# Optimization experiments

Measured on AMD Instinct MI355X. Metric: run time of the kernel, lower is better.

## Reference

```python
import jax, jax.numpy as jnp
import numpy as np
import math

CHANNELS = 128
NUM_NODES = 170
LENGTH = 12
BATCH = 128


def setup_inputs() -> dict:
    key = jax.random.key(0)
    k_x, k_es = jax.random.split(key)
    x = jax.random.normal(k_x, (BATCH, CHANNELS, NUM_NODES, LENGTH), dtype=jnp.float32)
    # xavier_uniform for E_s [channels, num_nodes]
    bound = math.sqrt(6.0 / (CHANNELS + NUM_NODES))
    E_s = jax.random.uniform(k_es, (CHANNELS, NUM_NODES), dtype=jnp.float32,
                             minval=-bound, maxval=bound)
    return {"x": x, "E_s": E_s}


def reference(x, E_s):
    # x: [B, C, N, T], E_s: [C, M] with M == N (num_nodes)
    # Note: the original also computes E_t = x * E_tod**2, which is dead code
    # (never used in the returned value), so it is omitted here.
    C = x.shape[1]
    # node embeddings: sum over channel and time -> [B, N, M]
    E_d = jnp.tanh(jnp.einsum('bcnt,cm->bnm', x, E_s))
    # node-node similarity: contract over the M (embedding) axis -> [B, N, N]
    scores = jax.nn.relu(jnp.einsum('bnm,bkm->bnk', E_d, E_d) / jnp.sqrt(jnp.float32(C)))
    A_adp = jax.nn.softmax(scores, axis=-1)  # [B, N, N]
    A_mean = A_adp.mean(axis=0)              # [N, N]
    return (A_mean > 0.5).astype(jnp.float32)
```

## Files before the change

### kernel.cpp

```cpp
#include <hip/hip_runtime.h>
#include <math.h>

#define NB 128
#define NC 128
#define NN 170
#define NT 12
#define MP 176
#define BSROW 196

#define XS_SZ  (NB * NC * MP)
#define ESP_SZ (NC * MP)
#define P_SZ   (NB * NN * MP)
#define ED_SZ  (NB * NN * MP)

__global__ __launch_bounds__(256) void k1_reduce_pad(const float* __restrict__ x,
                                                     const float* __restrict__ Es,
                                                     float* __restrict__ xs,
                                                     float* __restrict__ Esp) {
    if (blockIdx.x >= 10880) {
        int idx = (blockIdx.x - 10880) * 256 + threadIdx.x;
        if (idx < ESP_SZ) {
            int c = idx / MP, m = idx % MP;
            Esp[idx] = (m < NN) ? Es[c * NN + m] : 0.f;
        }
        return;
    }
    const int w    = blockIdx.x * 4 + (threadIdx.x >> 6);
    const int lane = threadIdx.x & 63;
    const float4* x4 = reinterpret_cast<const float4*>(x) + (size_t)w * 192;
    float4 f0 = x4[lane], f1 = x4[lane + 64], f2 = x4[lane + 128];
    float p0 = (f0.x + f0.y) + (f0.z + f0.w);
    float p1 = (f1.x + f1.y) + (f1.z + f1.w);
    float p2 = (f2.x + f2.y) + (f2.z + f2.w);
    float tot = 0.f;
    #pragma unroll
    for (int j = 0; j < 3; ++j) {
        int s = 3 * lane + j;
        int src = s & 63, reg = s >> 6;
        float a0 = __shfl(p0, src, 64);
        float a1 = __shfl(p1, src, 64);
        float a2 = __shfl(p2, src, 64);
        tot += (reg == 0) ? a0 : (reg == 1) ? a1 : a2;
    }
    int g  = w * 64 + lane;
    int bc = g / NN, n = g - bc * NN;
    xs[(size_t)bc * MP + n] = tot;
    if (n < MP - NN) xs[(size_t)bc * MP + NN + n] = 0.f;
}

__global__ __launch_bounds__(256) void k2_embed(const float* __restrict__ xs,
                                                const float* __restrict__ Esp,
                                                float* __restrict__ Ed) {
    const int b = blockIdx.y, n0 = blockIdx.x * 32;
    const int t = threadIdx.x, tx = t & 15, ty = t >> 4;
    __shared__ __align__(16) float As[16][36];
    __shared__ __align__(16) float Bs[16][BSROW];

    float acc[2][12] = {};
    for (int c0 = 0; c0 < NC; c0 += 16) {
        __syncthreads();
        if (t < 128) {
            int c = t >> 3, q = t & 7;
            float4 v = *reinterpret_cast<const float4*>(
                xs + ((size_t)(b * NC + c0 + c)) * MP + n0 + q * 4);
            *reinterpret_cast<float4*>(&As[c][q * 4]) = v;
        }
        #pragma unroll
        for (int it = 0; it < 3; ++it) {
            int idx = t + it * 256;
            int c = idx / 48, mq = idx - c * 48;
            float4 v = make_float4(0.f, 0.f, 0.f, 0.f);
            if (mq < 44)
                v = *reinterpret_cast<const float4*>(Esp + (c0 + c) * MP + mq * 4);
            *reinterpret_cast<float4*>(&Bs[c][mq * 4]) = v;
        }
        __syncthreads();
        #pragma unroll
        for (int cc = 0; cc < 16; ++cc) {
            float2 av = *reinterpret_cast<const float2*>(&As[cc][ty * 2]);
            float a[2] = {av.x, av.y};
            float bb[12];
            #pragma unroll
            for (int off = 0; off < 3; ++off) {
                float4 bv = *reinterpret_cast<const float4*>(&Bs[cc][tx * 4 + off * 64]);
                bb[off * 4 + 0] = bv.x; bb[off * 4 + 1] = bv.y;
                bb[off * 4 + 2] = bv.z; bb[off * 4 + 3] = bv.w;
            }
            #pragma unroll
            for (int ii = 0; ii < 2; ++ii)
                #pragma unroll
                for (int jj = 0; jj < 12; ++jj)
                    acc[ii][jj] = fmaf(a[ii], bb[jj], acc[ii][jj]);
        }
    }
    #pragma unroll
    for (int ii = 0; ii < 2; ++ii) {
        int n = n0 + ty * 2 + ii;
        if (n >= NN) continue;
        float* Erow = Ed + ((size_t)(b * NN + n)) * MP;
        #pragma unroll
        for (int off = 0; off < 3; ++off) {
            int m = tx * 4 + off * 64;
            if (m >= MP) continue;
            float4 v;
            v.x = tanhf(acc[ii][off * 4 + 0]);
            v.y = tanhf(acc[ii][off * 4 + 1]);
            v.z = tanhf(acc[ii][off * 4 + 2]);
            v.w = tanhf(acc[ii][off * 4 + 3]);
            *reinterpret_cast<float4*>(Erow + m) = v;
        }
    }
}

__global__ __launch_bounds__(256) void k3_scores(const float* __restrict__ Ed,
                                                 float* __restrict__ P) {
    const int b = blockIdx.y, r0 = blockIdx.x * 32;
    const int t = threadIdx.x, tx = t & 15, ty = t >> 4;
    __shared__ __align__(16) float Bs[16][BSROW];
    const float* __restrict__ Edb = Ed + (size_t)b * NN * MP;

    float acc[2][12] = {};
    for (int mc = 0; mc < MP; mc += 16) {
        __syncthreads();
        #pragma unroll
        for (int it = 0; it < 3; ++it) {
            int idx = t + it * 256;
            int k = idx >> 2, mq = idx & 3;
            float4 v = make_float4(0.f, 0.f, 0.f, 0.f);
            if (k < NN)
                v = *reinterpret_cast<const float4*>(Edb + (size_t)k * MP + mc + mq * 4);
            Bs[mq * 4 + 0][k] = v.x;
            Bs[mq * 4 + 1][k] = v.y;
            Bs[mq * 4 + 2][k] = v.z;
            Bs[mq * 4 + 3][k] = v.w;
        }
        __syncthreads();
        #pragma unroll
        for (int mm = 0; mm < 16; ++mm) {
            float2 av = *reinterpret_cast<const float2*>(&Bs[mm][r0 + ty * 2]);
            float a[2] = {av.x, av.y};
            float bb[12];
            #pragma unroll
            for (int off = 0; off < 3; ++off) {
                float4 bv = *reinterpret_cast<const float4*>(&Bs[mm][tx * 4 + off * 64]);
                bb[off * 4 + 0] = bv.x; bb[off * 4 + 1] = bv.y;
                bb[off * 4 + 2] = bv.z; bb[off * 4 + 3] = bv.w;
            }
            #pragma unroll
            for (int ii = 0; ii < 2; ++ii)
                #pragma unroll
                for (int jj = 0; jj < 12; ++jj)
                    acc[ii][jj] = fmaf(a[ii], bb[jj], acc[ii][jj]);
        }
    }

    const float scale = 0.08838834764831845f;
    #pragma unroll
    for (int ii = 0; ii < 2; ++ii) {
        int n = r0 + ty * 2 + ii;
        float vv[12];
        float mx = -1.f;
        #pragma unroll
        for (int jj = 0; jj < 12; ++jj) {
            int k = tx * 4 + (jj & 3) + (jj >> 2) * 64;
            bool valid = (k < NN);
            float v = fmaxf(acc[ii][jj] * scale, 0.f);
            vv[jj] = valid ? v : -1.f;
            mx = fmaxf(mx, vv[jj]);
        }
        #pragma unroll
        for (int off = 8; off; off >>= 1) mx = fmaxf(mx, __shfl_xor(mx, off, 64));
        float ex[12], sum = 0.f;
        #pragma unroll
        for (int jj = 0; jj < 12; ++jj) {
            int k = tx * 4 + (jj & 3) + (jj >> 2) * 64;
            float e = (k < NN) ? __expf(vv[jj] - mx) : 0.f;
            ex[jj] = e;
            sum += e;
        }
        #pragma unroll
        for (int off = 8; off; off >>= 1) sum += __shfl_xor(sum, off, 64);
        float inv = 1.f / sum;
        if (n < NN) {
            float* Pr = P + ((size_t)(b * NN + n)) * MP;
            #pragma unroll
            for (int off = 0; off < 3; ++off) {
                int k = tx * 4 + off * 64;
                if (k >= MP) continue;
                float4 v;
                v.x = ex[off * 4 + 0] * inv; v.y = ex[off * 4 + 1] * inv;
                v.z = ex[off * 4 + 2] * inv; v.w = ex[off * 4 + 3] * inv;
                *reinterpret_cast<float4*>(Pr + k) = v;
            }
        }
    }
}

__global__ __launch_bounds__(256) void k4a_partial(const float* __restrict__ P,
                                                   float* __restrict__ Pm) {
    int p = blockIdx.x * 256 + threadIdx.x;
    if (p >= NN * NN) return;
    int n = p / NN, k = p - n * NN;
    const float* base = P + (size_t)blockIdx.y * 16 * NN * MP + (size_t)n * MP + k;
    float s = 0.f;
    #pragma unroll
    for (int b = 0; b < 16; ++b) s += base[(size_t)b * NN * MP];
    Pm[blockIdx.y * (NN * NN) + p] = s;
}

__global__ __launch_bounds__(256) void k4b_thresh(const float* __restrict__ Pm,
                                                  float* __restrict__ out) {
    int p = blockIdx.x * 256 + threadIdx.x;
    if (p >= NN * NN) return;
    float s = 0.f;
    #pragma unroll
    for (int g = 0; g < 8; ++g) s += Pm[g * (NN * NN) + p];
    out[p] = (s * (1.f / 128.f) > 0.5f) ? 1.f : 0.f;
}

extern "C" void kernel_launch(void* const* d_in, const int* in_sizes, int n_in,
                              void* d_out, int out_size, void* d_ws, size_t ws_size,
                              hipStream_t stream) {
    const float* x  = (const float*)d_in[0];
    const float* Es = (const float*)d_in[1];
    float* out = (float*)d_out;
    float* wsf = (float*)d_ws;

    float* P   = wsf;
    float* xs  = wsf;
    float* Esp = wsf + XS_SZ;
    float* Ed  = wsf + P_SZ;
    float* Pm  = Ed;

    k1_reduce_pad<<<10968, 256, 0, stream>>>(x, Es, xs, Esp);
    k2_embed<<<dim3(6, 128), 256, 0, stream>>>(xs, Esp, Ed);
    k3_scores<<<dim3(6, 128), 256, 0, stream>>>(Ed, P);
    k4a_partial<<<dim3(113, 8), 256, 0, stream>>>(P, Pm);
    k4b_thresh<<<113, 256, 0, stream>>>(Pm, out);
}
```

Measured before the change: 250.7 us.

## Fuse batch mean into score kernel via atomics and use fast tanh

The score kernel no longer writes the full per-batch softmax matrix. It pre-scales each softmax value by 1/128 and atomically adds it into a single NN×NN accumulator, which the first kernel zeroes. This removes the large P write/read and the two-stage reduction, leaving a simple threshold kernel. The embedding kernel also swaps tanhf for an exp/rcp based approximation. The trade-offs are heavy atomic contention (128 batches adding into each cell) and nondeterministic summation order, which could flip outputs lying near the 0.5 threshold.

```diff
diff --git a/kernel.cpp b/kernel.cpp
--- a/kernel.cpp
+++ b/kernel.cpp
@@ -10,13 +10,25 @@
 
 #define XS_SZ  (NB * NC * MP)
 #define ESP_SZ (NC * MP)
-#define P_SZ   (NB * NN * MP)
 #define ED_SZ  (NB * NN * MP)
+#define PM_SZ  (NN * NN)
+
+__device__ __forceinline__ float fast_tanh(float x) {
+    float cx = fminf(fmaxf(x, -15.f), 15.f);
+    float e  = __expf(2.f * cx);
+    return (e - 1.f) * __builtin_amdgcn_rcpf(e + 1.f);
+}
 
 __global__ __launch_bounds__(256) void k1_reduce_pad(const float* __restrict__ x,
                                                      const float* __restrict__ Es,
                                                      float* __restrict__ xs,
-                                                     float* __restrict__ Esp) {
+                                                     float* __restrict__ Esp,
+                                                     float* __restrict__ Pm) {
+    if (blockIdx.x >= 10968) {
+        int idx = (blockIdx.x - 10968) * 256 + threadIdx.x;
+        if (idx < PM_SZ) Pm[idx] = 0.f;
+        return;
+    }
     if (blockIdx.x >= 10880) {
         int idx = (blockIdx.x - 10880) * 256 + threadIdx.x;
         if (idx < ESP_SZ) {
@@ -103,17 +115,17 @@
             int m = tx * 4 + off * 64;
             if (m >= MP) continue;
             float4 v;
-            v.x = tanhf(acc[ii][off * 4 + 0]);
-            v.y = tanhf(acc[ii][off * 4 + 1]);
-            v.z = tanhf(acc[ii][off * 4 + 2]);
-            v.w = tanhf(acc[ii][off * 4 + 3]);
+            v.x = fast_tanh(acc[ii][off * 4 + 0]);
+            v.y = fast_tanh(acc[ii][off * 4 + 1]);
+            v.z = fast_tanh(acc[ii][off * 4 + 2]);
+            v.w = fast_tanh(acc[ii][off * 4 + 3]);
             *reinterpret_cast<float4*>(Erow + m) = v;
         }
     }
 }
 
 __global__ __launch_bounds__(256) void k3_scores(const float* __restrict__ Ed,
-                                                 float* __restrict__ P) {
+                                                 float* __restrict__ Pm) {
     const int b = blockIdx.y, r0 = blockIdx.x * 32;
     const int t = threadIdx.x, tx = t & 15, ty = t >> 4;
     __shared__ __align__(16) float Bs[16][BSROW];
@@ -163,9 +175,8 @@
         #pragma unroll
         for (int jj = 0; jj < 12; ++jj) {
             int k = tx * 4 + (jj & 3) + (jj >> 2) * 64;
-            bool valid = (k < NN);
             float v = fmaxf(acc[ii][jj] * scale, 0.f);
-            vv[jj] = valid ? v : -1.f;
+            vv[jj] = (k < NN) ? v : -1.f;
             mx = fmaxf(mx, vv[jj]);
         }
         #pragma unroll
@@ -180,42 +191,23 @@
         }
         #pragma unroll
         for (int off = 8; off; off >>= 1) sum += __shfl_xor(sum, off, 64);
-        float inv = 1.f / sum;
+        float inv = (1.f / 128.f) / sum;
         if (n < NN) {
-            float* Pr = P + ((size_t)(b * NN + n)) * MP;
-            #pragma unroll
-            for (int off = 0; off < 3; ++off) {
-                int k = tx * 4 + off * 64;
-                if (k >= MP) continue;
-                float4 v;
-                v.x = ex[off * 4 + 0] * inv; v.y = ex[off * 4 + 1] * inv;
-                v.z = ex[off * 4 + 2] * inv; v.w = ex[off * 4 + 3] * inv;
-                *reinterpret_cast<float4*>(Pr + k) = v;
+            float* Pr = Pm + n * NN;
+            #pragma unroll
+            for (int jj = 0; jj < 12; ++jj) {
+                int k = tx * 4 + (jj & 3) + (jj >> 2) * 64;
+                if (k < NN) atomicAdd(Pr + k, ex[jj] * inv);
             }
         }
     }
 }
 
-__global__ __launch_bounds__(256) void k4a_partial(const float* __restrict__ P,
-                                                   float* __restrict__ Pm) {
+__global__ __launch_bounds__(256) void k4_thresh(const float* __restrict__ Pm,
+                                                 float* __restrict__ out) {
     int p = blockIdx.x * 256 + threadIdx.x;
-    if (p >= NN * NN) return;
-    int n = p / NN, k = p - n * NN;
-    const float* base = P + (size_t)blockIdx.y * 16 * NN * MP + (size_t)n * MP + k;
-    float s = 0.f;
-    #pragma unroll
-    for (int b = 0; b < 16; ++b) s += base[(size_t)b * NN * MP];
-    Pm[blockIdx.y * (NN * NN) + p] = s;
-}
-
-__global__ __launch_bounds__(256) void k4b_thresh(const float* __restrict__ Pm,
-                                                  float* __restrict__ out) {
-    int p = blockIdx.x * 256 + threadIdx.x;
-    if (p >= NN * NN) return;
-    float s = 0.f;
-    #pragma unroll
-    for (int g = 0; g < 8; ++g) s += Pm[g * (NN * NN) + p];
-    out[p] = (s * (1.f / 128.f) > 0.5f) ? 1.f : 0.f;
+    if (p >= PM_SZ) return;
+    out[p] = (Pm[p] > 0.5f) ? 1.f : 0.f;
 }
 
 extern "C" void kernel_launch(void* const* d_in, const int* in_sizes, int n_in,
@@ -226,15 +218,13 @@
     float* out = (float*)d_out;
     float* wsf = (float*)d_ws;
 
-    float* P   = wsf;
     float* xs  = wsf;
     float* Esp = wsf + XS_SZ;
-    float* Ed  = wsf + P_SZ;
-    float* Pm  = Ed;
-
-    k1_reduce_pad<<<10968, 256, 0, stream>>>(x, Es, xs, Esp);
+    float* Ed  = wsf + XS_SZ + ESP_SZ;
+    float* Pm  = wsf + XS_SZ + ESP_SZ + ED_SZ;
+
+    k1_reduce_pad<<<11081, 256, 0, stream>>>(x, Es, xs, Esp, Pm);
     k2_embed<<<dim3(6, 128), 256, 0, stream>>>(xs, Esp, Ed);
-    k3_scores<<<dim3(6, 128), 256, 0, stream>>>(Ed, P);
-    k4a_partial<<<dim3(113, 8), 256, 0, stream>>>(P, Pm);
-    k4b_thresh<<<113, 256, 0, stream>>>(Pm, out);
-}
+    k3_scores<<<dim3(6, 128), 256, 0, stream>>>(Ed, Pm);
+    k4_thresh<<<113, 256, 0, stream>>>(Pm, out);
+}
```

Result: slower. 316.2 us (+26.1%).

## Fuse time-axis reduction of x into embedding GEMM and use fast tanh

Applied to the files above, without the earlier changes.

Drops the separate reduce kernel that summed x over time into a padded xs buffer. The embedding kernel now loads the 12 time values per (b,c,n) straight from x and sums them while filling its shared tile. This saves the xs write and re-read and one launch. It also swaps tanhf for an exp/rcp-based tanh and gives each buffer its own slot in the workspace. In exchange, each thread's x loads are strided by 48 bytes across nodes, so global loads are less coalesced than the old float4 streaming reduction, and only 768 blocks now read the 100MB input.

```diff
diff --git a/kernel.cpp b/kernel.cpp
--- a/kernel.cpp
+++ b/kernel.cpp
@@ -8,47 +8,27 @@
 #define MP 176
 #define BSROW 196
 
-#define XS_SZ  (NB * NC * MP)
 #define ESP_SZ (NC * MP)
+#define ED_SZ  (NB * NN * MP)
 #define P_SZ   (NB * NN * MP)
-#define ED_SZ  (NB * NN * MP)
-
-__global__ __launch_bounds__(256) void k1_reduce_pad(const float* __restrict__ x,
-                                                     const float* __restrict__ Es,
-                                                     float* __restrict__ xs,
-                                                     float* __restrict__ Esp) {
-    if (blockIdx.x >= 10880) {
-        int idx = (blockIdx.x - 10880) * 256 + threadIdx.x;
-        if (idx < ESP_SZ) {
-            int c = idx / MP, m = idx % MP;
-            Esp[idx] = (m < NN) ? Es[c * NN + m] : 0.f;
-        }
-        return;
-    }
-    const int w    = blockIdx.x * 4 + (threadIdx.x >> 6);
-    const int lane = threadIdx.x & 63;
-    const float4* x4 = reinterpret_cast<const float4*>(x) + (size_t)w * 192;
-    float4 f0 = x4[lane], f1 = x4[lane + 64], f2 = x4[lane + 128];
-    float p0 = (f0.x + f0.y) + (f0.z + f0.w);
-    float p1 = (f1.x + f1.y) + (f1.z + f1.w);
-    float p2 = (f2.x + f2.y) + (f2.z + f2.w);
-    float tot = 0.f;
-    #pragma unroll
-    for (int j = 0; j < 3; ++j) {
-        int s = 3 * lane + j;
-        int src = s & 63, reg = s >> 6;
-        float a0 = __shfl(p0, src, 64);
-        float a1 = __shfl(p1, src, 64);
-        float a2 = __shfl(p2, src, 64);
-        tot += (reg == 0) ? a0 : (reg == 1) ? a1 : a2;
-    }
-    int g  = w * 64 + lane;
-    int bc = g / NN, n = g - bc * NN;
-    xs[(size_t)bc * MP + n] = tot;
-    if (n < MP - NN) xs[(size_t)bc * MP + NN + n] = 0.f;
-}
-
-__global__ __launch_bounds__(256) void k2_embed(const float* __restrict__ xs,
+#define PM_SZ  (8 * NN * NN)
+
+__device__ __forceinline__ float fast_tanh(float x) {
+    float cx = fminf(fmaxf(x, -15.f), 15.f);
+    float e  = __expf(2.f * cx);
+    return (e - 1.f) * __builtin_amdgcn_rcpf(e + 1.f);
+}
+
+__global__ __launch_bounds__(256) void k0_pad_es(const float* __restrict__ Es,
+                                                 float* __restrict__ Esp) {
+    int idx = blockIdx.x * 256 + threadIdx.x;
+    if (idx < ESP_SZ) {
+        int c = idx / MP, m = idx % MP;
+        Esp[idx] = (m < NN) ? Es[c * NN + m] : 0.f;
+    }
+}
+
+__global__ __launch_bounds__(256) void k2_fused(const float* __restrict__ x,
                                                 const float* __restrict__ Esp,
                                                 float* __restrict__ Ed) {
     const int b = blockIdx.y, n0 = blockIdx.x * 32;
@@ -59,11 +39,23 @@
     float acc[2][12] = {};
     for (int c0 = 0; c0 < NC; c0 += 16) {
         __syncthreads();
-        if (t < 128) {
-            int c = t >> 3, q = t & 7;
-            float4 v = *reinterpret_cast<const float4*>(
-                xs + ((size_t)(b * NC + c0 + c)) * MP + n0 + q * 4);
-            *reinterpret_cast<float4*>(&As[c][q * 4]) = v;
+        {
+            int c  = t >> 4;
+            int nn = (t & 15) * 2;
+            #pragma unroll
+            for (int u = 0; u < 2; ++u) {
+                int n = n0 + nn + u;
+                float s = 0.f;
+                if (n < NN) {
+                    const float4* p = reinterpret_cast<const float4*>(
+                        x + ((size_t)((b * NC + c0 + c) * NN) + n) * NT);
+                    float4 f0 = p[0], f1 = p[1], f2 = p[2];
+                    s = ((f0.x + f0.y) + (f0.z + f0.w))
+                      + ((f1.x + f1.y) + (f1.z + f1.w))
+                      + ((f2.x + f2.y) + (f2.z + f2.w));
+                }
+                As[c][nn + u] = s;
+            }
         }
         #pragma unroll
         for (int it = 0; it < 3; ++it) {
@@ -103,10 +95,10 @@
             int m = tx * 4 + off * 64;
             if (m >= MP) continue;
             float4 v;
-            v.x = tanhf(acc[ii][off * 4 + 0]);
-            v.y = tanhf(acc[ii][off * 4 + 1]);
-            v.z = tanhf(acc[ii][off * 4 + 2]);
-            v.w = tanhf(acc[ii][off * 4 + 3]);
+            v.x = fast_tanh(acc[ii][off * 4 + 0]);
+            v.y = fast_tanh(acc[ii][off * 4 + 1]);
+            v.z = fast_tanh(acc[ii][off * 4 + 2]);
+            v.w = fast_tanh(acc[ii][off * 4 + 3]);
             *reinterpret_cast<float4*>(Erow + m) = v;
         }
     }
@@ -163,9 +155,8 @@
         #pragma unroll
         for (int jj = 0; jj < 12; ++jj) {
             int k = tx * 4 + (jj & 3) + (jj >> 2) * 64;
-            bool valid = (k < NN);
             float v = fmaxf(acc[ii][jj] * scale, 0.f);
-            vv[jj] = valid ? v : -1.f;
+            vv[jj] = (k < NN) ? v : -1.f;
             mx = fmaxf(mx, vv[jj]);
         }
         #pragma unroll
@@ -226,14 +217,13 @@
     float* out = (float*)d_out;
     float* wsf = (float*)d_ws;
 
-    float* P   = wsf;
-    float* xs  = wsf;
-    float* Esp = wsf + XS_SZ;
-    float* Ed  = wsf + P_SZ;
-    float* Pm  = Ed;
-
-    k1_reduce_pad<<<10968, 256, 0, stream>>>(x, Es, xs, Esp);
-    k2_embed<<<dim3(6, 128), 256, 0, stream>>>(xs, Esp, Ed);
+    float* Esp = wsf;
+    float* Ed  = wsf + ESP_SZ;
+    float* P   = wsf + ESP_SZ + ED_SZ;
+    float* Pm  = wsf + ESP_SZ + ED_SZ + P_SZ;
+
+    k0_pad_es<<<88, 256, 0, stream>>>(Es, Esp);
+    k2_fused<<<dim3(6, 128), 256, 0, stream>>>(x, Esp, Ed);
     k3_scores<<<dim3(6, 128), 256, 0, stream>>>(Ed, P);
     k4a_partial<<<dim3(113, 8), 256, 0, stream>>>(P, Pm);
     k4b_thresh<<<113, 256, 0, stream>>>(Pm, out);
```

New measurement: 243.7 us. 2.8% less time.
